# Kernel optimization log

Hardware: AMD Instinct MI355X
Metric: run time of the kernel (lower is better)

Reference implementation:

```python
import jax, jax.numpy as jnp
import numpy as np


def dct_matrix(T):
    # Orthonormal DCT-II matrix: y = D @ x  (torch_dct.dct(..., norm='ortho'))
    n = jnp.arange(T, dtype=jnp.float32)
    k = jnp.arange(T, dtype=jnp.float32)[:, None]
    D = jnp.cos(jnp.pi * (n + 0.5) * k / T) * np.sqrt(2.0 / T)
    D = D.at[0].mul(1.0 / np.sqrt(2.0))
    return D.astype(jnp.float32)


def setup_inputs() -> dict:
    key = jax.random.key(0)
    k1, k2, k3 = jax.random.split(key, 3)
    B, C, T, H, W = 8, 64, 16, 64, 64
    text_dim = 768
    r = jax.random.normal(k1, (B, C, T, H, W), dtype=jnp.float32)
    E_txt = jax.random.normal(k2, (B, text_dim), dtype=jnp.float32)
    Wf = jax.random.normal(k3, (C * T, text_dim), dtype=jnp.float32) * 0.02
    bf = jnp.zeros((C * T,), dtype=jnp.float32)
    return {"r": r, "E_txt": E_txt, "Wf": Wf, "bf": bf}


def reference(r, E_txt, Wf, bf):
    B, C, T, H, W = r.shape
    D = dct_matrix(T)  # (T, T), orthonormal so IDCT = D.T
    # DCT-II along the T axis (avoids materializing permuted copies)
    r_freq = jnp.einsum('bcthw,kt->bckhw', r, D)
    # sigmoid-gated per-(B,C,T) frequency modulation
    w = jax.nn.sigmoid((E_txt @ Wf.T + bf).reshape(B, C, T, 1, 1))
    mod = r_freq * w
    # inverse DCT (DCT-III ortho) along the frequency axis back to T
    r_out = jnp.einsum('bckhw,kt->bcthw', mod, D)
    return r_out
```

## Files before the change

### kernel.cpp

```cpp
#include <hip/hip_runtime.h>
#include <math.h>


#define HW4 1024

typedef float f4 __attribute__((ext_vector_type(4)));

__global__ __launch_bounds__(256) void gate_kernel(
    const float* __restrict__ E,
    const float* __restrict__ Wf,
    const float* __restrict__ bf,
    float* __restrict__ wout)
{
    const int wave = threadIdx.x >> 6;
    const int lane = threadIdx.x & 63;
    const int ct   = blockIdx.x * 4 + wave;

    const float4* W4 = (const float4*)(Wf) + ct * 192;
    const float4* E4 = (const float4*)E;

    float acc[8];
#pragma unroll
    for (int b = 0; b < 8; ++b) acc[b] = 0.f;

#pragma unroll
    for (int j = 0; j < 3; ++j) {
        float4 a = W4[j * 64 + lane];
#pragma unroll
        for (int b = 0; b < 8; ++b) {
            float4 e = E4[b * 192 + j * 64 + lane];
            acc[b] = fmaf(a.x, e.x, acc[b]);
            acc[b] = fmaf(a.y, e.y, acc[b]);
            acc[b] = fmaf(a.z, e.z, acc[b]);
            acc[b] = fmaf(a.w, e.w, acc[b]);
        }
    }
#pragma unroll
    for (int off = 32; off >= 1; off >>= 1) {
#pragma unroll
        for (int b = 0; b < 8; ++b)
            acc[b] += __shfl_xor(acc[b], off, 64);
    }
    const float bias = bf[ct];
#pragma unroll
    for (int b = 0; b < 8; ++b) {
        if (lane == b) {
            float s = acc[b] + bias;
            wout[b * 1024 + ct] = 1.0f / (1.0f + expf(-s));
        }
    }
}

__global__ __launch_bounds__(256, 4) void mod_kernel(
    const float* __restrict__ r,
    const float* __restrict__ wbuf,
    float* __restrict__ out)
{
    __shared__ float Dl[16][16];
    __shared__ float wv[16];
    __shared__ __align__(16) float Ms[256];

    const int tid   = threadIdx.x;
    const int wave  = tid >> 6;
    const int lane  = tid & 63;
    const int bc    = blockIdx.x >> 2;
    const int chunk = (blockIdx.x & 3) * 4 + wave;

    const size_t base = (size_t)bc * (16 * 4096);
    const f4* rp = (const f4*)(r + base);
    f4*       op = (f4*)(out + base);
    const int col = chunk * 64 + lane;

    f4 xb[4];
#pragma unroll
    for (int k = 0; k < 4; ++k)
        xb[k] = __builtin_nontemporal_load(&rp[k * HW4 + col]);

    {
        int k = tid >> 4, n = tid & 15;
        float v = (k == 0) ? 0.25f
                           : cospif((n + 0.5f) * (float)k * (1.0f / 16.0f)) * 0.35355339059327373f;
        Dl[k][n] = v;
        if (tid < 16) wv[tid] = wbuf[bc * 16 + tid];
    }
    __syncthreads();
    {
        int i = tid >> 4, j = tid & 15;
        float s = 0.f;
#pragma unroll
        for (int k = 0; k < 16; ++k)
            s = fmaf(Dl[k][i] * wv[k], Dl[k][j], s);
        Ms[j * 16 + i] = s;
    }
    __syncthreads();

    f4 y[16];
#pragma unroll
    for (int t = 0; t < 16; ++t)
        y[t] = (f4){0.f, 0.f, 0.f, 0.f};

#pragma unroll
    for (int k = 0; k < 16; ++k) {
        f4 xk = xb[k & 3];
        if (k + 4 < 16)
            xb[k & 3] = __builtin_nontemporal_load(&rp[(k + 4) * HW4 + col]);
        const f4* Mk = (const f4*)(Ms + k * 16);
#pragma unroll
        for (int t4 = 0; t4 < 4; ++t4) {
            f4 m = Mk[t4];
            y[4 * t4 + 0].x = fmaf(m.x, xk.x, y[4 * t4 + 0].x);
            y[4 * t4 + 0].y = fmaf(m.x, xk.y, y[4 * t4 + 0].y);
            y[4 * t4 + 0].z = fmaf(m.x, xk.z, y[4 * t4 + 0].z);
            y[4 * t4 + 0].w = fmaf(m.x, xk.w, y[4 * t4 + 0].w);
            y[4 * t4 + 1].x = fmaf(m.y, xk.x, y[4 * t4 + 1].x);
            y[4 * t4 + 1].y = fmaf(m.y, xk.y, y[4 * t4 + 1].y);
            y[4 * t4 + 1].z = fmaf(m.y, xk.z, y[4 * t4 + 1].z);
            y[4 * t4 + 1].w = fmaf(m.y, xk.w, y[4 * t4 + 1].w);
            y[4 * t4 + 2].x = fmaf(m.z, xk.x, y[4 * t4 + 2].x);
            y[4 * t4 + 2].y = fmaf(m.z, xk.y, y[4 * t4 + 2].y);
            y[4 * t4 + 2].z = fmaf(m.z, xk.z, y[4 * t4 + 2].z);
            y[4 * t4 + 2].w = fmaf(m.z, xk.w, y[4 * t4 + 2].w);
            y[4 * t4 + 3].x = fmaf(m.w, xk.x, y[4 * t4 + 3].x);
            y[4 * t4 + 3].y = fmaf(m.w, xk.y, y[4 * t4 + 3].y);
            y[4 * t4 + 3].z = fmaf(m.w, xk.z, y[4 * t4 + 3].z);
            y[4 * t4 + 3].w = fmaf(m.w, xk.w, y[4 * t4 + 3].w);
        }
    }

#pragma unroll
    for (int t = 0; t < 16; ++t)
        __builtin_nontemporal_store(y[t], &op[t * HW4 + col]);
}

extern "C" void kernel_launch(void* const* d_in, const int* in_sizes, int n_in,
                              void* d_out, int out_size, void* d_ws, size_t ws_size,
                              hipStream_t stream) {
    const float* r  = (const float*)d_in[0];
    const float* E  = (const float*)d_in[1];
    const float* Wf = (const float*)d_in[2];
    const float* bf = (const float*)d_in[3];
    float* out = (float*)d_out;
    float* w   = (float*)d_ws;

    gate_kernel<<<256, 256, 0, stream>>>(E, Wf, bf, w);
    mod_kernel <<<2048, 256, 0, stream>>>(r, w, out);
}
```

Baseline: 240.3 us.

## Fuse sigmoid gate GEMV into modulation kernel and deepen load prefetch

Removes the separate gate kernel launch and its workspace round-trip. Each block now computes its 16 gate values itself: 16-lane groups form dot products over Wf rows and E, reduced with shuffles. The prefetch depth of r loads is raised from 4 to 8 rows to keep more memory requests in flight. The cost is redundant GEMV work, since each (b,c) gate is recomputed by 4 blocks, along with higher register pressure.

New measurement: 240.8 us. No clear change (+0.2%).

```diff
diff --git a/kernel.cpp b/kernel.cpp
--- a/kernel.cpp
+++ b/kernel.cpp
@@ -6,54 +6,11 @@
 
 typedef float f4 __attribute__((ext_vector_type(4)));
 
-__global__ __launch_bounds__(256) void gate_kernel(
+__global__ __launch_bounds__(256, 4) void fused_kernel(
+    const float* __restrict__ r,
     const float* __restrict__ E,
     const float* __restrict__ Wf,
     const float* __restrict__ bf,
-    float* __restrict__ wout)
-{
-    const int wave = threadIdx.x >> 6;
-    const int lane = threadIdx.x & 63;
-    const int ct   = blockIdx.x * 4 + wave;
-
-    const float4* W4 = (const float4*)(Wf) + ct * 192;
-    const float4* E4 = (const float4*)E;
-
-    float acc[8];
-#pragma unroll
-    for (int b = 0; b < 8; ++b) acc[b] = 0.f;
-
-#pragma unroll
-    for (int j = 0; j < 3; ++j) {
-        float4 a = W4[j * 64 + lane];
-#pragma unroll
-        for (int b = 0; b < 8; ++b) {
-            float4 e = E4[b * 192 + j * 64 + lane];
-            acc[b] = fmaf(a.x, e.x, acc[b]);
-            acc[b] = fmaf(a.y, e.y, acc[b]);
-            acc[b] = fmaf(a.z, e.z, acc[b]);
-            acc[b] = fmaf(a.w, e.w, acc[b]);
-        }
-    }
-#pragma unroll
-    for (int off = 32; off >= 1; off >>= 1) {
-#pragma unroll
-        for (int b = 0; b < 8; ++b)
-            acc[b] += __shfl_xor(acc[b], off, 64);
-    }
-    const float bias = bf[ct];
-#pragma unroll
-    for (int b = 0; b < 8; ++b) {
-        if (lane == b) {
-            float s = acc[b] + bias;
-            wout[b * 1024 + ct] = 1.0f / (1.0f + expf(-s));
-        }
-    }
-}
-
-__global__ __launch_bounds__(256, 4) void mod_kernel(
-    const float* __restrict__ r,
-    const float* __restrict__ wbuf,
     float* __restrict__ out)
 {
     __shared__ float Dl[16][16];
@@ -65,32 +22,61 @@
     const int lane  = tid & 63;
     const int bc    = blockIdx.x >> 2;
     const int chunk = (blockIdx.x & 3) * 4 + wave;
+    const int b     = bc >> 6;
+    const int c     = bc & 63;
+    const int krow  = tid >> 4;
+    const int sub   = tid & 15;
 
     const size_t base = (size_t)bc * (16 * 4096);
     const f4* rp = (const f4*)(r + base);
     f4*       op = (f4*)(out + base);
     const int col = chunk * 64 + lane;
 
-    f4 xb[4];
+    const f4* W4 = (const f4*)Wf + (size_t)(c * 16 + krow) * 192 + sub;
+    const f4* E4 = (const f4*)E + b * 192 + sub;
+    float p0 = 0.f, p1 = 0.f, p2 = 0.f, p3 = 0.f;
 #pragma unroll
-    for (int k = 0; k < 4; ++k)
+    for (int j = 0; j < 12; j += 4) {
+        f4 w0 = W4[16*(j+0)], e0 = E4[16*(j+0)];
+        f4 w1 = W4[16*(j+1)], e1 = E4[16*(j+1)];
+        f4 w2 = W4[16*(j+2)], e2 = E4[16*(j+2)];
+        f4 w3 = W4[16*(j+3)], e3 = E4[16*(j+3)];
+        p0 = fmaf(w0.x,e0.x,p0); p0 = fmaf(w0.y,e0.y,p0);
+        p0 = fmaf(w0.z,e0.z,p0); p0 = fmaf(w0.w,e0.w,p0);
+        p1 = fmaf(w1.x,e1.x,p1); p1 = fmaf(w1.y,e1.y,p1);
+        p1 = fmaf(w1.z,e1.z,p1); p1 = fmaf(w1.w,e1.w,p1);
+        p2 = fmaf(w2.x,e2.x,p2); p2 = fmaf(w2.y,e2.y,p2);
+        p2 = fmaf(w2.z,e2.z,p2); p2 = fmaf(w2.w,e2.w,p2);
+        p3 = fmaf(w3.x,e3.x,p3); p3 = fmaf(w3.y,e3.y,p3);
+        p3 = fmaf(w3.z,e3.z,p3); p3 = fmaf(w3.w,e3.w,p3);
+    }
+
+    f4 xb[8];
+#pragma unroll
+    for (int k = 0; k < 8; ++k)
         xb[k] = __builtin_nontemporal_load(&rp[k * HW4 + col]);
 
-    {
-        int k = tid >> 4, n = tid & 15;
-        float v = (k == 0) ? 0.25f
-                           : cospif((n + 0.5f) * (float)k * (1.0f / 16.0f)) * 0.35355339059327373f;
-        Dl[k][n] = v;
-        if (tid < 16) wv[tid] = wbuf[bc * 16 + tid];
+    float p = (p0 + p1) + (p2 + p3);
+    p += __shfl_xor(p, 1, 64);
+    p += __shfl_xor(p, 2, 64);
+    p += __shfl_xor(p, 4, 64);
+    p += __shfl_xor(p, 8, 64);
+
+    Dl[krow][sub] = (krow == 0)
+        ? 0.25f
+        : cospif((sub + 0.5f) * (float)krow * (1.0f / 16.0f)) * 0.35355339059327373f;
+    if (sub == 0) {
+        float s = p + bf[c * 16 + krow];
+        wv[krow] = 1.0f / (1.0f + expf(-s));
     }
     __syncthreads();
+
     {
-        int i = tid >> 4, j = tid & 15;
         float s = 0.f;
 #pragma unroll
         for (int k = 0; k < 16; ++k)
-            s = fmaf(Dl[k][i] * wv[k], Dl[k][j], s);
-        Ms[j * 16 + i] = s;
+            s = fmaf(Dl[k][krow] * wv[k], Dl[k][sub], s);
+        Ms[sub * 16 + krow] = s;
     }
     __syncthreads();
 
@@ -101,9 +87,9 @@
 
 #pragma unroll
     for (int k = 0; k < 16; ++k) {
-        f4 xk = xb[k & 3];
-        if (k + 4 < 16)
-            xb[k & 3] = __builtin_nontemporal_load(&rp[(k + 4) * HW4 + col]);
+        f4 xk = xb[k & 7];
+        if (k + 8 < 16)
+            xb[k & 7] = __builtin_nontemporal_load(&rp[(k + 8) * HW4 + col]);
         const f4* Mk = (const f4*)(Ms + k * 16);
 #pragma unroll
         for (int t4 = 0; t4 < 4; ++t4) {
@@ -140,8 +126,6 @@
     const float* Wf = (const float*)d_in[2];
     const float* bf = (const float*)d_in[3];
     float* out = (float*)d_out;
-    float* w   = (float*)d_ws;
 
-    gate_kernel<<<256, 256, 0, stream>>>(E, Wf, bf, w);
-    mod_kernel <<<2048, 256, 0, stream>>>(r, w, out);
+    fused_kernel<<<2048, 256, 0, stream>>>(r, E, Wf, bf, out);
 }
```
